# Optimization experiments

Hardware: AMD Instinct MI355X
Metric: run time of the kernel (lower is better)

The kernel has to match this reference:

```python
import jax, jax.numpy as jnp
import numpy as np

B, N, D = 8, 65536, 192
EPS = 1e-5  # matches cal_norm_batch eps

# corner offsets (i,j,k) in {0,1}^3, shape [2,2,2,3]
_OFFS = np.stack(np.meshgrid(np.arange(2), np.arange(2), np.arange(2), indexing='ij'), -1)


def setup_inputs() -> dict:
    key = jax.random.key(0)
    k1, k2 = jax.random.split(key)
    pss = jax.random.uniform(k1, (B, 3, N), jnp.float32)          # points in [0,1]^3
    sdf_grids = jax.random.normal(k2, (B, D, D, D), jnp.float32)  # per-batch SDF grids
    first = jnp.zeros((B, 3), jnp.float32)                        # grid origin
    coef = jnp.full((B, 3), float(D - 2), jnp.float32)            # 1/voxel_size
    max_limit = jnp.full((B, 3), float(D - 2), jnp.float32)       # keeps idx+1 <= D-1
    return {"pss": pss, "sdf_grids": sdf_grids, "first": first, "coef": coef, "max_limit": max_limit}


def reference(pss, sdf_grids, first, coef, max_limit):
    p = jnp.transpose(pss, (0, 2, 1))  # [B,N,3]
    f_full = jnp.clip(jnp.minimum((p - first[:, None, :]) * coef[:, None, :],
                                  max_limit[:, None, :]), 0.0)
    base = jnp.floor(f_full)
    frac = f_full - base               # [B,N,3] trilinear fractions
    idx8 = base.astype(jnp.int32)[:, :, None, None, None, :] + jnp.asarray(_OFFS, jnp.int32)  # [B,N,2,2,2,3]
    # 8-corner gather, per-batch grid
    corners = jax.vmap(lambda g, I: g[I[..., 0], I[..., 1], I[..., 2]])(sdf_grids, idx8)  # [B,N,2,2,2]
    fx, fy, fz = frac[..., 0], frac[..., 1], frac[..., 2]
    wx = jnp.stack([1 - fx, fx], -1)  # [B,N,2]
    wy = jnp.stack([1 - fy, fy], -1)
    wz = jnp.stack([1 - fz, fz], -1)
    # trilinear SDF value
    dss = jnp.einsum('bnijk,bni,bnj,bnk->bn', corners, wx, wy, wz)
    # finite-difference normals (interp3d_batch with grad=True along each axis)
    n_z = jnp.einsum('bnij,bni,bnj->bn', corners[..., 1] - corners[..., 0], wx, wy)
    n_y = jnp.einsum('bnik,bni,bnk->bn', corners[:, :, :, 1, :] - corners[:, :, :, 0, :], wx, wz)
    n_x = jnp.einsum('bnjk,bnj,bnk->bn', corners[:, :, 1] - corners[:, :, 0], wy, wz)
    n = jnp.stack([n_x, n_y, n_z], -1)  # [B,N,3]
    nss = n / jnp.clip(jnp.linalg.norm(n, axis=-1, keepdims=True), EPS)
    loss = -jnp.sum(jnp.minimum(dss, 0.0))
    return dss, nss, loss
```

## Files before the change

### kernel.cpp

```cpp
#include <hip/hip_runtime.h>

#define BB 8
#define NN 65536
#define DD 192
#define EPSV 1e-5f

#define CAX 24
#define CELLS_B (CAX * CAX * CAX)
#define TCELLS (BB * CELLS_B)
#define NPTS (BB * NN)
#define SCAN_BLOCKS (TCELLS / 256)

#define SORT0 (TCELLS + 512)

__device__ __forceinline__ void point_setup(
    const float* __restrict__ pss, const float* __restrict__ first,
    const float* __restrict__ coef, const float* __restrict__ maxl,
    int t, int& b, float& fx, float& fy, float& fz,
    int& bx, int& by, int& bz, int& key)
{
    b = t >> 16;
    const int n = t & (NN - 1);
    const float* pb = pss + (size_t)b * 3 * NN + n;
    const float px = pb[0];
    const float py = pb[NN];
    const float pz = pb[2 * NN];

    const float Fx = fmaxf(fminf((px - first[3*b+0]) * coef[3*b+0], maxl[3*b+0]), 0.0f);
    const float Fy = fmaxf(fminf((py - first[3*b+1]) * coef[3*b+1], maxl[3*b+1]), 0.0f);
    const float Fz = fmaxf(fminf((pz - first[3*b+2]) * coef[3*b+2], maxl[3*b+2]), 0.0f);

    bx = (int)floorf(Fx);
    by = (int)floorf(Fy);
    bz = (int)floorf(Fz);
    fx = Fx - (float)bx;
    fy = Fy - (float)by;
    fz = Fz - (float)bz;

    key = ((b * CAX + (bx >> 3)) * CAX + (by >> 3)) * CAX + (bz >> 3);
}

__global__ __launch_bounds__(256) void hist_kernel(
    const float* __restrict__ pss, const float* __restrict__ first,
    const float* __restrict__ coef, const float* __restrict__ maxl,
    unsigned* __restrict__ hist)
{
    const int t = blockIdx.x * blockDim.x + threadIdx.x;
    int b, bx, by, bz, key; float fx, fy, fz;
    point_setup(pss, first, coef, maxl, t, b, fx, fy, fz, bx, by, bz, key);
    atomicAdd(&hist[key], 1u);
}

__global__ __launch_bounds__(256) void scan1_kernel(unsigned* __restrict__ hist,
                                                    unsigned* __restrict__ bsum)
{
    __shared__ unsigned s[256];
    const int tid = threadIdx.x;
    const int i = blockIdx.x * 256 + tid;
    const unsigned v = hist[i];
    s[tid] = v;
    __syncthreads();
    #pragma unroll
    for (int off = 1; off < 256; off <<= 1) {
        unsigned tv = (tid >= off) ? s[tid - off] : 0u;
        __syncthreads();
        s[tid] += tv;
        __syncthreads();
    }
    hist[i] = s[tid] - v;
    if (tid == 255) bsum[blockIdx.x] = s[255];
}

__global__ __launch_bounds__(512) void scan2_kernel(unsigned* __restrict__ bsum)
{
    __shared__ unsigned s[512];
    const int tid = threadIdx.x;
    const unsigned v = (tid < SCAN_BLOCKS) ? bsum[tid] : 0u;
    s[tid] = v;
    __syncthreads();
    #pragma unroll
    for (int off = 1; off < 512; off <<= 1) {
        unsigned tv = (tid >= off) ? s[tid - off] : 0u;
        __syncthreads();
        s[tid] += tv;
        __syncthreads();
    }
    if (tid < SCAN_BLOCKS) bsum[tid] = s[tid] - v;
}

__global__ __launch_bounds__(256) void scan3_kernel(unsigned* __restrict__ hist,
                                                    const unsigned* __restrict__ bsum)
{
    const int i = blockIdx.x * 256 + threadIdx.x;
    hist[i] += bsum[blockIdx.x];
}

__global__ __launch_bounds__(256) void scatter_kernel(
    const float* __restrict__ pss, const float* __restrict__ first,
    const float* __restrict__ coef, const float* __restrict__ maxl,
    unsigned* __restrict__ cursor,
    float* __restrict__ sfx, float* __restrict__ sfy, float* __restrict__ sfz,
    unsigned* __restrict__ sbase, unsigned* __restrict__ sorig)
{
    const int t = blockIdx.x * blockDim.x + threadIdx.x;
    int b, bx, by, bz, key; float fx, fy, fz;
    point_setup(pss, first, coef, maxl, t, b, fx, fy, fz, bx, by, bz, key);
    const unsigned pos = atomicAdd(&cursor[key], 1u);
    sfx[pos] = fx;
    sfy[pos] = fy;
    sfz[pos] = fz;
    sbase[pos] = ((unsigned)b << 24) | ((unsigned)bx << 16) | ((unsigned)by << 8) | (unsigned)bz;
    sorig[pos] = (unsigned)t;
}

__global__ __launch_bounds__(256) void main_kernel(
    const float* __restrict__ grid,
    const float* __restrict__ sfx, const float* __restrict__ sfy,
    const float* __restrict__ sfz, const unsigned* __restrict__ sbase,
    const unsigned* __restrict__ sorig,
    float* __restrict__ dss, float* __restrict__ nss, float* __restrict__ loss)
{
    const int i = blockIdx.x * blockDim.x + threadIdx.x;

    const float fx = sfx[i];
    const float fy = sfy[i];
    const float fz = sfz[i];
    const unsigned pk = sbase[i];
    const int b  = (int)(pk >> 24);
    const int bx = (int)((pk >> 16) & 255u);
    const int by = (int)((pk >> 8) & 255u);
    const int bz = (int)(pk & 255u);

    const float* g = grid + (size_t)b * DD * DD * DD
                          + ((size_t)bx * DD + by) * DD + bz;
    const float c000 = g[0];
    const float c001 = g[1];
    const float c010 = g[DD];
    const float c011 = g[DD + 1];
    const float c100 = g[DD * DD];
    const float c101 = g[DD * DD + 1];
    const float c110 = g[DD * DD + DD];
    const float c111 = g[DD * DD + DD + 1];

    const float wx0 = 1.0f - fx, wx1 = fx;
    const float wy0 = 1.0f - fy, wy1 = fy;
    const float wz0 = 1.0f - fz, wz1 = fz;

    const float d00 = wz0 * c000 + wz1 * c001;
    const float d01 = wz0 * c010 + wz1 * c011;
    const float d10 = wz0 * c100 + wz1 * c101;
    const float d11 = wz0 * c110 + wz1 * c111;
    const float d0  = wy0 * d00 + wy1 * d01;
    const float d1  = wy0 * d10 + wy1 * d11;
    const float dv  = wx0 * d0 + wx1 * d1;

    const float nz = wx0 * (wy0 * (c001 - c000) + wy1 * (c011 - c010))
                   + wx1 * (wy0 * (c101 - c100) + wy1 * (c111 - c110));
    const float ny = wx0 * (wz0 * (c010 - c000) + wz1 * (c011 - c001))
                   + wx1 * (wz0 * (c110 - c100) + wz1 * (c111 - c101));
    const float nx = wy0 * (wz0 * (c100 - c000) + wz1 * (c101 - c001))
                   + wy1 * (wz0 * (c110 - c010) + wz1 * (c111 - c011));

    const float nrm = sqrtf(nx * nx + ny * ny + nz * nz);
    const float inv = 1.0f / fmaxf(nrm, EPSV);

    const unsigned t = sorig[i];
    dss[t] = dv;
    float* np_ = nss + (size_t)t * 3;
    np_[0] = nx * inv;
    np_[1] = ny * inv;
    np_[2] = nz * inv;

    float lp = fminf(dv, 0.0f);
    #pragma unroll
    for (int off = 32; off > 0; off >>= 1)
        lp += __shfl_down(lp, off, 64);
    __shared__ float wsum[4];
    const int wid = threadIdx.x >> 6;
    if ((threadIdx.x & 63) == 0) wsum[wid] = lp;
    __syncthreads();
    if (threadIdx.x == 0)
        atomicAdd(loss, -(wsum[0] + wsum[1] + wsum[2] + wsum[3]));
}

extern "C" void kernel_launch(void* const* d_in, const int* in_sizes, int n_in,
                              void* d_out, int out_size, void* d_ws, size_t ws_size,
                              hipStream_t stream) {
    const float* pss   = (const float*)d_in[0];
    const float* grid  = (const float*)d_in[1];
    const float* first = (const float*)d_in[2];
    const float* coef  = (const float*)d_in[3];
    const float* maxl  = (const float*)d_in[4];

    float* out  = (float*)d_out;
    float* dss  = out;
    float* nss  = out + (size_t)BB * NN;
    float* loss = out + (size_t)4 * BB * NN;

    unsigned* ws    = (unsigned*)d_ws;
    unsigned* hist  = ws;
    unsigned* bsum  = ws + TCELLS;
    float*    sfx   = (float*)(ws + SORT0 + (size_t)0 * NPTS);
    float*    sfy   = (float*)(ws + SORT0 + (size_t)1 * NPTS);
    float*    sfz   = (float*)(ws + SORT0 + (size_t)2 * NPTS);
    unsigned* sbase =          ws + SORT0 + (size_t)3 * NPTS;
    unsigned* sorig =          ws + SORT0 + (size_t)4 * NPTS;

    hipMemsetAsync(hist, 0, (size_t)TCELLS * sizeof(unsigned), stream);
    hipMemsetAsync(loss, 0, sizeof(float), stream);

    const int threads = 256;
    const int pblocks = NPTS / threads;

    hist_kernel<<<pblocks, threads, 0, stream>>>(pss, first, coef, maxl, hist);
    scan1_kernel<<<SCAN_BLOCKS, 256, 0, stream>>>(hist, bsum);
    scan2_kernel<<<1, 512, 0, stream>>>(bsum);
    scan3_kernel<<<SCAN_BLOCKS, 256, 0, stream>>>(hist, bsum);
    scatter_kernel<<<pblocks, threads, 0, stream>>>(pss, first, coef, maxl, hist,
                                                    sfx, sfy, sfz, sbase, sorig);
    main_kernel<<<pblocks, threads, 0, stream>>>(grid, sfx, sfy, sfz, sbase, sorig,
                                                 dss, nss, loss);
}
```

Measured before the change: 376.7 us.

## Pack sorted records into float4 and move output scatter to a gather pass

The scatter kernel now writes one packed float4 record per point, holding the fractions and the packed base index, at its sorted slot. It also records each point's sorted rank at its original index. The main kernel writes its result coalesced as a float4 in sorted order, and a new reorder kernel gathers by rank into the original-order dss and nss outputs. This swaps five scattered 4-byte writes and scattered output stores for vector writes and a coalesced-output gather, at the cost of an extra kernel launch and an intermediate buffer pass.

```diff
diff --git a/kernel.cpp b/kernel.cpp
--- a/kernel.cpp
+++ b/kernel.cpp
@@ -11,7 +11,9 @@
 #define NPTS (BB * NN)
 #define SCAN_BLOCKS (TCELLS / 256)
 
-#define SORT0 (TCELLS + 512)
+#define RANK0 (TCELLS + 512)
+#define REC0  (RANK0 + NPTS)
+#define RES0  (REC0 + 4 * NPTS)
 
 __device__ __forceinline__ void point_setup(
     const float* __restrict__ pss, const float* __restrict__ first,
@@ -99,33 +101,30 @@
     const float* __restrict__ pss, const float* __restrict__ first,
     const float* __restrict__ coef, const float* __restrict__ maxl,
     unsigned* __restrict__ cursor,
-    float* __restrict__ sfx, float* __restrict__ sfy, float* __restrict__ sfz,
-    unsigned* __restrict__ sbase, unsigned* __restrict__ sorig)
+    float4* __restrict__ rec,
+    unsigned* __restrict__ rank)
 {
     const int t = blockIdx.x * blockDim.x + threadIdx.x;
     int b, bx, by, bz, key; float fx, fy, fz;
     point_setup(pss, first, coef, maxl, t, b, fx, fy, fz, bx, by, bz, key);
     const unsigned pos = atomicAdd(&cursor[key], 1u);
-    sfx[pos] = fx;
-    sfy[pos] = fy;
-    sfz[pos] = fz;
-    sbase[pos] = ((unsigned)b << 24) | ((unsigned)bx << 16) | ((unsigned)by << 8) | (unsigned)bz;
-    sorig[pos] = (unsigned)t;
+    const unsigned base = ((unsigned)b << 24) | ((unsigned)bx << 16)
+                        | ((unsigned)by << 8) | (unsigned)bz;
+    rec[pos] = make_float4(fx, fy, fz, __uint_as_float(base));
+    rank[t] = pos;
 }
 
 __global__ __launch_bounds__(256) void main_kernel(
     const float* __restrict__ grid,
-    const float* __restrict__ sfx, const float* __restrict__ sfy,
-    const float* __restrict__ sfz, const unsigned* __restrict__ sbase,
-    const unsigned* __restrict__ sorig,
-    float* __restrict__ dss, float* __restrict__ nss, float* __restrict__ loss)
+    const float4* __restrict__ rec,
+    float4* __restrict__ res,
+    float* __restrict__ loss)
 {
     const int i = blockIdx.x * blockDim.x + threadIdx.x;
 
-    const float fx = sfx[i];
-    const float fy = sfy[i];
-    const float fz = sfz[i];
-    const unsigned pk = sbase[i];
+    const float4 r = rec[i];
+    const float fx = r.x, fy = r.y, fz = r.z;
+    const unsigned pk = __float_as_uint(r.w);
     const int b  = (int)(pk >> 24);
     const int bx = (int)((pk >> 16) & 255u);
     const int by = (int)((pk >> 8) & 255u);
@@ -164,12 +163,7 @@
     const float nrm = sqrtf(nx * nx + ny * ny + nz * nz);
     const float inv = 1.0f / fmaxf(nrm, EPSV);
 
-    const unsigned t = sorig[i];
-    dss[t] = dv;
-    float* np_ = nss + (size_t)t * 3;
-    np_[0] = nx * inv;
-    np_[1] = ny * inv;
-    np_[2] = nz * inv;
+    res[i] = make_float4(dv, nx * inv, ny * inv, nz * inv);
 
     float lp = fminf(dv, 0.0f);
     #pragma unroll
@@ -183,6 +177,20 @@
         atomicAdd(loss, -(wsum[0] + wsum[1] + wsum[2] + wsum[3]));
 }
 
+__global__ __launch_bounds__(256) void reorder_kernel(
+    const unsigned* __restrict__ rank,
+    const float4* __restrict__ res,
+    float* __restrict__ dss, float* __restrict__ nss)
+{
+    const int t = blockIdx.x * blockDim.x + threadIdx.x;
+    const float4 v = res[rank[t]];
+    dss[t] = v.x;
+    float* np_ = nss + (size_t)t * 3;
+    np_[0] = v.y;
+    np_[1] = v.z;
+    np_[2] = v.w;
+}
+
 extern "C" void kernel_launch(void* const* d_in, const int* in_sizes, int n_in,
                               void* d_out, int out_size, void* d_ws, size_t ws_size,
                               hipStream_t stream) {
@@ -197,14 +205,12 @@
     float* nss  = out + (size_t)BB * NN;
     float* loss = out + (size_t)4 * BB * NN;
 
-    unsigned* ws    = (unsigned*)d_ws;
-    unsigned* hist  = ws;
-    unsigned* bsum  = ws + TCELLS;
-    float*    sfx   = (float*)(ws + SORT0 + (size_t)0 * NPTS);
-    float*    sfy   = (float*)(ws + SORT0 + (size_t)1 * NPTS);
-    float*    sfz   = (float*)(ws + SORT0 + (size_t)2 * NPTS);
-    unsigned* sbase =          ws + SORT0 + (size_t)3 * NPTS;
-    unsigned* sorig =          ws + SORT0 + (size_t)4 * NPTS;
+    unsigned* ws   = (unsigned*)d_ws;
+    unsigned* hist = ws;
+    unsigned* bsum = ws + TCELLS;
+    unsigned* rank = ws + RANK0;
+    float4*   rec  = (float4*)(ws + REC0);
+    float4*   res  = (float4*)(ws + RES0);
 
     hipMemsetAsync(hist, 0, (size_t)TCELLS * sizeof(unsigned), stream);
     hipMemsetAsync(loss, 0, sizeof(float), stream);
@@ -217,7 +223,7 @@
     scan2_kernel<<<1, 512, 0, stream>>>(bsum);
     scan3_kernel<<<SCAN_BLOCKS, 256, 0, stream>>>(hist, bsum);
     scatter_kernel<<<pblocks, threads, 0, stream>>>(pss, first, coef, maxl, hist,
-                                                    sfx, sfy, sfz, sbase, sorig);
-    main_kernel<<<pblocks, threads, 0, stream>>>(grid, sfx, sfy, sfz, sbase, sorig,
-                                                 dss, nss, loss);
-}
+                                                    rec, rank);
+    main_kernel<<<pblocks, threads, 0, stream>>>(grid, rec, res, loss);
+    reorder_kernel<<<pblocks, threads, 0, stream>>>(rank, res, dss, nss);
+}
```

Result: no change. 375.9 us (-0.2%).
